# Performance work log

Measured on AMD Instinct MI355X. Metric: run time of the kernel, lower is better.

Reference implementation:

```python
import jax, jax.numpy as jnp
import numpy as np

# ---- Cl(4,1) geometric-product Cayley table (32 blades, metric diag(+,+,+,+,-)) ----
def _build_gp_map():
    metric = [1.0, 1.0, 1.0, 1.0, -1.0]  # e1..e4 square to +1, e5 squares to -1
    gp = np.zeros((32, 32, 32), dtype=np.float32)
    for a in range(32):          # blade a as a bitmask over 5 generators
        for b in range(32):
            # sign from reordering generators into canonical order
            swaps = 0
            t = a >> 1
            while t:
                swaps += bin(t & b).count('1')
                t >>= 1
            sign = -1.0 if (swaps & 1) else 1.0
            # sign from contracted (repeated) generators via the metric
            common = a & b
            for i in range(5):
                if common & (1 << i):
                    sign *= metric[i]
            gp[a, b, a ^ b] = sign  # e_a * e_b = sign * e_{a xor b}
    return gp

GP_MAP = _build_gp_map()  # [32, 32, 32], highly sparse (one nonzero per (a,b))
EPS = 1e-6

B, S, IN, OUT = 2, 1024, 256, 256

def setup_inputs() -> dict:
    key = jax.random.key(0)
    k1, k2 = jax.random.split(key)
    x = jax.random.normal(k1, (B, S, IN, 32), dtype=jnp.float32)
    std = 1.0 / float(np.sqrt(IN * 32))  # grade-aware Xavier scale from reset_parameters
    weight = jax.random.normal(k2, (OUT, IN, 32), dtype=jnp.float32) * std
    return {"x": x, "weight": weight}

def normalize_cl41(mv):
    # normalize each multivector by its coefficient magnitude over the 32 lanes
    norm = jnp.sqrt(jnp.sum(mv * mv, axis=-1, keepdims=True) + EPS)
    return mv / norm

def reference(x, weight):
    gp = jnp.asarray(GP_MAP, dtype=x.dtype)
    # W_op[o,i,l,k] = sum_j weight[o,i,j] * gp[j,l,k]
    W_op = jnp.einsum('oij,jlk->oilk', weight, gp)
    # out[b,s,o,k] = sum_{i,l} x[b,s,i,l] * W_op[o,i,l,k]
    out = jnp.einsum('bsil,oilk->bsok', x, W_op)
    return normalize_cl41(out)
```

## Files before the change

### kernel.cpp

```cpp
#include <hip/hip_runtime.h>
#include <hip/hip_bf16.h>
#include <stdint.h>

typedef _Float16 f16;
typedef __attribute__((ext_vector_type(8))) _Float16 f16x8;
typedef __attribute__((ext_vector_type(4))) float f32x4;

#define M_DIM 2048
#define K_FULL 8192
#define M2 8192
#define K2 2048
#define N2 2048
#define BM 128
#define BN 128
#define BK 32
#define PSTR 132

struct CMat { int re[4][4]; int im[4][4]; };

constexpr CMat cmul(const CMat& A, const CMat& B) {
  CMat C{};
  for (int r = 0; r < 4; ++r)
    for (int c = 0; c < 4; ++c) {
      int re = 0, im = 0;
      for (int t = 0; t < 4; ++t) {
        re += A.re[r][t] * B.re[t][c] - A.im[r][t] * B.im[t][c];
        im += A.re[r][t] * B.im[t][c] + A.im[r][t] * B.re[t][c];
      }
      C.re[r][c] = re; C.im[r][c] = im;
    }
  return C;
}

constexpr int gp_sign_ct(int a, int b) {
  int sw = 0;
  for (int t = a >> 1; t; t >>= 1) {
    int x = t & b;
    while (x) { sw += x & 1; x >>= 1; }
  }
  int s = (sw & 1) ? -1 : 1;
  if ((a & b) & 16) s = -s;
  return s;
}

struct Tables {
  int8_t f_idx[32][4]; int8_t f_sgn[32][4];
  int8_t g_idx[32][4]; int8_t g_sgn[32][4];
  bool ok;
};

constexpr Tables make_tables() {
  CMat G[5] = {
    { {{0,0,0,1},{0,0,1,0},{0,1,0,0},{1,0,0,0}},
      {{0,0,0,0},{0,0,0,0},{0,0,0,0},{0,0,0,0}} },
    { {{0,0,0,0},{0,0,0,0},{0,0,0,0},{0,0,0,0}},
      {{0,0,0,-1},{0,0,1,0},{0,-1,0,0},{1,0,0,0}} },
    { {{0,0,1,0},{0,0,0,-1},{1,0,0,0},{0,-1,0,0}},
      {{0,0,0,0},{0,0,0,0},{0,0,0,0},{0,0,0,0}} },
    { {{0,0,0,0},{0,0,0,0},{0,0,0,0},{0,0,0,0}},
      {{0,0,-1,0},{0,0,0,-1},{1,0,0,0},{0,1,0,0}} },
    { {{0,0,0,0},{0,0,0,0},{0,0,0,0},{0,0,0,0}},
      {{1,0,0,0},{0,1,0,0},{0,0,-1,0},{0,0,0,-1}} } };
  CMat ID{ {{1,0,0,0},{0,1,0,0},{0,0,1,0},{0,0,0,1}},
           {{0,0,0,0},{0,0,0,0},{0,0,0,0},{0,0,0,0}} };
  CMat U[32] = {};
  for (int A = 0; A < 32; ++A) {
    CMat u = ID;
    for (int b = 0; b < 5; ++b) if (A & (1 << b)) u = cmul(u, G[b]);
    U[A] = u;
  }
  bool ok = true;
  for (int a = 0; a < 32; ++a)
    for (int b = 0; b < 32; ++b) {
      CMat P = cmul(U[a], U[b]);
      int s = gp_sign_ct(a, b);
      const CMat& T = U[a ^ b];
      for (int r = 0; r < 4; ++r)
        for (int c = 0; c < 4; ++c)
          if (P.re[r][c] != s * T.re[r][c] || P.im[r][c] != s * T.im[r][c]) ok = false;
    }
  Tables t{};
  int cnt[32] = {};
  for (int A = 0; A < 32; ++A) {
    int n = 0;
    for (int r = 0; r < 4; ++r)
      for (int c = 0; c < 4; ++c) {
        int vr = U[A].re[r][c], vi = U[A].im[r][c];
        if (vr) {
          int s = (r * 4 + c) * 2;
          if (n < 4 && cnt[s] < 4) {
            t.g_idx[A][n] = (int8_t)s; t.g_sgn[A][n] = (int8_t)vr;
            t.f_idx[s][cnt[s]] = (int8_t)A; t.f_sgn[s][cnt[s]] = (int8_t)vr;
            cnt[s]++;
          } else ok = false;
          n++;
        }
        if (vi) {
          int s = (r * 4 + c) * 2 + 1;
          if (n < 4 && cnt[s] < 4) {
            t.g_idx[A][n] = (int8_t)s; t.g_sgn[A][n] = (int8_t)vi;
            t.f_idx[s][cnt[s]] = (int8_t)A; t.f_sgn[s][cnt[s]] = (int8_t)vi;
            cnt[s]++;
          } else ok = false;
          n++;
        }
      }
    if (n != 4) ok = false;
  }
  for (int s = 0; s < 32; ++s) if (cnt[s] != 4) ok = false;
  t.ok = ok;
  return t;
}

constexpr Tables HT = make_tables();
static_assert(HT.ok, "Cl(4,1) -> M(4,C) homomorphism check FAILED");


__device__ __forceinline__ void async16(const f16* g, f16* l) {
  __builtin_amdgcn_global_load_lds(
      (const __attribute__((address_space(1))) uint32_t*)g,
      (__attribute__((address_space(3))) uint32_t*)l,
      16, 0, 0);
}

__device__ __forceinline__ float gp_sign_rt(int a, int b) {
  int sw = 0;
  for (int t = a >> 1; t; t >>= 1) sw += __popc(t & b);
  float s = (sw & 1) ? -1.0f : 1.0f;
  if ((a & b) & 16) s = -s;
  return s;
}

__global__ __launch_bounds__(256) void fwd_x_kernel(const float* __restrict__ x,
                                                    f16* __restrict__ Ag) {
  __shared__ float xs[256 * 33];
  const int m = blockIdx.x, t = threadIdx.x;
  const float4* src = (const float4*)(x + (size_t)m * 8192);
#pragma unroll
  for (int c = t; c < 2048; c += 256) {
    float4 v = src[c];
    float* d = xs + (c >> 3) * 33 + ((c & 7) << 2);
    d[0] = v.x; d[1] = v.y; d[2] = v.z; d[3] = v.w;
  }
  __syncthreads();
  const float* xv = xs + t * 33;
  float sv[32];
#pragma unroll
  for (int s = 0; s < 32; ++s)
    sv[s] = (float)HT.f_sgn[s][0] * xv[HT.f_idx[s][0]]
          + (float)HT.f_sgn[s][1] * xv[HT.f_idx[s][1]]
          + (float)HT.f_sgn[s][2] * xv[HT.f_idx[s][2]]
          + (float)HT.f_sgn[s][3] * xv[HT.f_idx[s][3]];
#pragma unroll
  for (int c = 0; c < 4; ++c) {
    f16x8 h;
#pragma unroll
    for (int e = 0; e < 8; ++e) {
      int tt = e >> 1, p = e & 1;
      h[e] = (f16)sv[tt * 8 + c * 2 + p];
    }
    *(f16x8*)(Ag + ((size_t)(m * 4 + c)) * K2 + t * 8) = h;
  }
}

__global__ __launch_bounds__(256) void fwd_w_kernel(const float* __restrict__ w,
                                                    f16* __restrict__ Bt) {
  __shared__ float xs[256 * 33];
  const int o = blockIdx.x, t = threadIdx.x;
  const float4* src = (const float4*)(w + (size_t)o * 8192);
#pragma unroll
  for (int c = t; c < 2048; c += 256) {
    float4 v = src[c];
    float* d = xs + (c >> 3) * 33 + ((c & 7) << 2);
    d[0] = v.x; d[1] = v.y; d[2] = v.z; d[3] = v.w;
  }
  __syncthreads();
  const float* wv = xs + t * 33;
  float sv[32];
#pragma unroll
  for (int s = 0; s < 32; ++s)
    sv[s] = (float)HT.f_sgn[s][0] * wv[HT.f_idx[s][0]]
          + (float)HT.f_sgn[s][1] * wv[HT.f_idx[s][1]]
          + (float)HT.f_sgn[s][2] * wv[HT.f_idx[s][2]]
          + (float)HT.f_sgn[s][3] * wv[HT.f_idx[s][3]];
#pragma unroll
  for (int r = 0; r < 4; ++r)
#pragma unroll
    for (int q = 0; q < 2; ++q) {
      f16x8 h;
#pragma unroll
      for (int e = 0; e < 8; ++e) {
        int tt = e >> 1, p = e & 1;
        float re = sv[(r * 4 + tt) * 2], im = sv[(r * 4 + tt) * 2 + 1];
        float v = (q == 0) ? (p == 0 ? re : -im) : (p == 0 ? im : re);
        h[e] = (f16)v;
      }
      *(f16x8*)(Bt + ((size_t)(o * 8 + r * 2 + q)) * K2 + t * 8) = h;
    }
}

__global__ __launch_bounds__(256) void gemm_fused_kernel(const f16* __restrict__ A,
                                                         const f16* __restrict__ Bw,
                                                         float* __restrict__ out) {
  __shared__ __align__(16) char smem[64 * PSTR * 4];
  f16* As = (f16*)smem;
  f16* Bs = (f16*)(smem + BM * BK * 2);
  float* ps = (float*)smem;
  const int t = threadIdx.x;
  const int wave = t >> 6, lane = t & 63;
  const int wr = wave >> 1, wc = wave & 1;
  const int g = lane >> 4, lc = lane & 15;
  const int m0 = blockIdx.y * BM, n0 = blockIdx.x * BN;

  f32x4 acc[4][4];
#pragma unroll
  for (int i = 0; i < 4; ++i)
#pragma unroll
    for (int j = 0; j < 4; ++j) {
      acc[i][j][0] = 0.f; acc[i][j][1] = 0.f; acc[i][j][2] = 0.f; acc[i][j][3] = 0.f;
    }

  const f16* agp[2]; const f16* bgp[2];
  f16* alp[2]; f16* blp[2];
#pragma unroll
  for (int q = 0; q < 2; ++q) {
    int chunk = (q << 8) + (wave << 6) + lane;
    int row = chunk >> 2;
    int gk = ((chunk & 3) ^ ((row >> 1) & 3)) << 3;
    agp[q] = A  + (size_t)(m0 + row) * K2 + gk;
    bgp[q] = Bw + (size_t)(n0 + row) * K2 + gk;
    alp[q] = As + (q << 11) + (wave << 9);
    blp[q] = Bs + (q << 11) + (wave << 9);
  }

  const int swz = (lc >> 1) & 3;
  int aoff[4], boff[4];
#pragma unroll
  for (int i = 0; i < 4; ++i) {
    aoff[i] = ((wr << 6) + (i << 4) + lc) * BK + ((g ^ swz) << 3);
    boff[i] = ((wc << 6) + (i << 4) + lc) * BK + ((g ^ swz) << 3);
  }

  for (int kk = 0; kk < K2; kk += BK) {
    async16(agp[0] + kk, alp[0]);
    async16(agp[1] + kk, alp[1]);
    async16(bgp[0] + kk, blp[0]);
    async16(bgp[1] + kk, blp[1]);
    __syncthreads();

    f16x8 av[4], bv[4];
#pragma unroll
    for (int i = 0; i < 4; ++i) av[i] = *(const f16x8*)(As + aoff[i]);
#pragma unroll
    for (int i = 0; i < 4; ++i) bv[i] = *(const f16x8*)(Bs + boff[i]);
#pragma unroll
    for (int tm = 0; tm < 4; ++tm)
#pragma unroll
      for (int tn = 0; tn < 4; ++tn)
        acc[tm][tn] = __builtin_amdgcn_mfma_f32_16x16x32_f16(av[tm], bv[tn],
                                                             acc[tm][tn], 0, 0, 0);
    __syncthreads();
  }

#pragma unroll
  for (int half = 0; half < 2; ++half) {
    if (half) __syncthreads();
    if (wr == half) {
#pragma unroll
      for (int tm = 0; tm < 4; ++tm) {
        int rowl = (tm << 4) + (g << 2);
#pragma unroll
        for (int tn = 0; tn < 4; ++tn) {
          int col = (wc << 6) + (tn << 4) + lc;
#pragma unroll
          for (int r = 0; r < 4; ++r)
            ps[(rowl + r) * PSTR + col] = acc[tm][tn][r];
        }
      }
    }
    __syncthreads();

    const int mh = t >> 4, oh = t & 15;
    float yv[4][8];
#pragma unroll
    for (int c = 0; c < 4; ++c) {
      const float* row = ps + (mh * 4 + c) * PSTR + oh * 8;
      *(float4*)&yv[c][0] = *(const float4*)row;
      *(float4*)&yv[c][4] = *(const float4*)(row + 4);
    }
    float ss = 0.f;
#pragma unroll
    for (int c = 0; c < 4; ++c)
#pragma unroll
      for (int j = 0; j < 8; ++j) ss += yv[c][j] * yv[c][j];
    float inv = rsqrtf(0.25f * ss + 1e-6f);

    float ov[32];
#pragma unroll
    for (int k = 0; k < 32; ++k) {
      float v = 0.f;
#pragma unroll
      for (int j = 0; j < 4; ++j) {
        int s = HT.g_idx[k][j];
        int cell = s >> 1;
        int rr = cell >> 2, cc = cell & 3, pp = s & 1;
        float sgn = (float)HT.g_sgn[k][j];
        v += sgn * yv[cc][rr * 2 + pp];
      }
      ov[k] = v * 0.25f * inv;
    }
    int m = (m0 >> 2) + (half << 4) + mh;
    int o = (n0 >> 3) + oh;
    float* op = out + (size_t)m * 8192 + o * 32;
#pragma unroll
    for (int q = 0; q < 8; ++q)
      *(float4*)(op + q * 4) = make_float4(ov[q * 4], ov[q * 4 + 1],
                                           ov[q * 4 + 2], ov[q * 4 + 3]);
  }
}

__global__ __launch_bounds__(256) void naive_vl_kernel(const float* __restrict__ x,
                                                       const float* __restrict__ w,
                                                       float* __restrict__ out) {
  __shared__ float xs[8192];
  __shared__ float sgt[1024];
  int m = blockIdx.x, o0 = blockIdx.y << 3;
  int t = threadIdx.x;
  for (int i = t; i < 1024; i += 256) {
    int kk = i >> 5, ll = i & 31;
    sgt[i] = gp_sign_rt(kk ^ ll, ll);
  }
  const float4* xr = (const float4*)(x + (size_t)m * K_FULL);
  float4* xs4 = (float4*)xs;
  for (int i = t; i < 2048; i += 256) xs4[i] = xr[i];
  __syncthreads();
  int k = t & 31, ol = t >> 5;
  int o = o0 + ol;
  const float* wrow = w + (size_t)o * K_FULL;
  float acc = 0.f;
  for (int l = 0; l < 32; ++l) {
    float s = sgt[(k << 5) + l];
    const float* wp = wrow + (k ^ l);
    const float* xp = xs + l;
    float part = 0.f;
#pragma unroll 8
    for (int i = 0; i < 256; ++i) part += xp[i << 5] * wp[i << 5];
    acc += part * s;
  }
  float ss = acc * acc;
  for (int msk = 1; msk < 32; msk <<= 1) ss += __shfl_xor(ss, msk, 32);
  out[((size_t)m * 256 + o) * 32 + k] = acc * rsqrtf(ss + 1e-6f);
}

extern "C" void kernel_launch(void* const* d_in, const int* in_sizes, int n_in,
                              void* d_out, int out_size, void* d_ws, size_t ws_size,
                              hipStream_t stream) {
  const float* x = (const float*)d_in[0];
  const float* w = (const float*)d_in[1];
  float* out = (float*)d_out;

  size_t agE = (size_t)M2 * K2;
  size_t btE = (size_t)N2 * K2;
  size_t need = (agE + btE) * sizeof(f16);

  if (ws_size >= need) {
    f16* Ag = (f16*)d_ws;
    f16* Bt = Ag + agE;
    fwd_x_kernel<<<dim3(M_DIM), dim3(256), 0, stream>>>(x, Ag);
    fwd_w_kernel<<<dim3(256), dim3(256), 0, stream>>>(w, Bt);
    gemm_fused_kernel<<<dim3(N2 / BN, M2 / BM), dim3(256), 0, stream>>>(Ag, Bt, out);
  } else {
    naive_vl_kernel<<<dim3(M_DIM, 32), dim3(256), 0, stream>>>(x, w, out);
  }
}
```

Before: 233.1 us.

## Rewrite GEMM as 256x256 double-buffered MFMA pipeline with block swizzle

Grows the fused GEMM tile to 256x256x64 with 512 threads and 8 waves, and double-buffers the 128KB LDS so the global-to-LDS async loads for tile t+2 overlap the MFMAs on tile t. Manual vmcnt waits, raw s_barrier, setprio and sched_barrier phases interleave LDS fragment reads with the MFMA groups. A 1D grid with a block-index swizzle is meant to improve L2 reuse. The aim is to cut global traffic per flop and hide load latency. In exchange it needs far more LDS and registers per block, which risks low occupancy, and the hand-written sync is fragile.

```diff
diff --git a/kernel.cpp b/kernel.cpp
--- a/kernel.cpp
+++ b/kernel.cpp
@@ -11,10 +11,11 @@
 #define M2 8192
 #define K2 2048
 #define N2 2048
-#define BM 128
-#define BN 128
-#define BK 32
-#define PSTR 132
+#define BM 256
+#define BN 256
+#define BK 64
+#define NT (K2 / BK)
+#define PSTR 260
 
 struct CMat { int re[4][4]; int im[4][4]; };
 
@@ -114,7 +115,7 @@
 
 constexpr Tables HT = make_tables();
 static_assert(HT.ok, "Cl(4,1) -> M(4,C) homomorphism check FAILED");
-
+static_assert((NT & 1) == 0, "buffer parity requires even tile count");
 
 __device__ __forceinline__ void async16(const f16* g, f16* l) {
   __builtin_amdgcn_global_load_lds(
@@ -130,6 +131,10 @@
   if ((a & b) & 16) s = -s;
   return s;
 }
+
+#define FENCE() asm volatile("" ::: "memory")
+#define BARRIER() do { FENCE(); __builtin_amdgcn_s_barrier(); FENCE(); } while (0)
+#define WAIT_VM(N) asm volatile("s_waitcnt vmcnt(" #N ")" ::: "memory")
 
 __global__ __launch_bounds__(256) void fwd_x_kernel(const float* __restrict__ x,
                                                     f16* __restrict__ Ag) {
@@ -199,88 +204,161 @@
     }
 }
 
-__global__ __launch_bounds__(256) void gemm_fused_kernel(const f16* __restrict__ A,
-                                                         const f16* __restrict__ Bw,
-                                                         float* __restrict__ out) {
-  __shared__ __align__(16) char smem[64 * PSTR * 4];
-  f16* As = (f16*)smem;
-  f16* Bs = (f16*)(smem + BM * BK * 2);
-  float* ps = (float*)smem;
+__global__ __launch_bounds__(512, 2) void gemm_fused_kernel(const f16* __restrict__ A,
+                                                            const f16* __restrict__ Bw,
+                                                            float* __restrict__ out) {
+  __shared__ __align__(16) char smem[131072];
   const int t = threadIdx.x;
-  const int wave = t >> 6, lane = t & 63;
-  const int wr = wave >> 1, wc = wave & 1;
+  const int w = t >> 6, lane = t & 63;
+  const int wr = w >> 2, wc = w & 3;
   const int g = lane >> 4, lc = lane & 15;
-  const int m0 = blockIdx.y * BM, n0 = blockIdx.x * BN;
-
-  f32x4 acc[4][4];
-#pragma unroll
-  for (int i = 0; i < 4; ++i)
+
+  const int bid = blockIdx.x;
+  const int swzb = (bid & 7) * 32 + (bid >> 3);
+  const int by = swzb >> 3, bx = swzb & 7;
+  const int m0 = by * BM, n0 = bx * BN;
+
+  const int srow = lane >> 3;
+  const int schk = (lane & 7) ^ srow;
+  const f16* ga0 = A  + (size_t)(m0 + w * 8 + srow) * K2 + schk * 8;
+  const f16* gb0 = Bw + (size_t)(n0 + w * 8 + srow) * K2 + schk * 8;
+  const int lw = w << 10;
+
+  const int cks0 = (g ^ (lc & 7)) << 4;
+  const int cks1 = ((4 | g) ^ (lc & 7)) << 4;
+  const int arow = (wr << 14) + (lc << 7);
+  const int brow = 32768 + (wc << 13) + (lc << 7);
+
+  f32x4 acc[8][4];
+#pragma unroll
+  for (int i = 0; i < 8; ++i)
 #pragma unroll
     for (int j = 0; j < 4; ++j) {
       acc[i][j][0] = 0.f; acc[i][j][1] = 0.f; acc[i][j][2] = 0.f; acc[i][j][3] = 0.f;
     }
 
-  const f16* agp[2]; const f16* bgp[2];
-  f16* alp[2]; f16* blp[2];
-#pragma unroll
-  for (int q = 0; q < 2; ++q) {
-    int chunk = (q << 8) + (wave << 6) + lane;
-    int row = chunk >> 2;
-    int gk = ((chunk & 3) ^ ((row >> 1) & 3)) << 3;
-    agp[q] = A  + (size_t)(m0 + row) * K2 + gk;
-    bgp[q] = Bw + (size_t)(n0 + row) * K2 + gk;
-    alp[q] = As + (q << 11) + (wave << 9);
-    blp[q] = Bs + (q << 11) + (wave << 9);
-  }
-
-  const int swz = (lc >> 1) & 3;
-  int aoff[4], boff[4];
-#pragma unroll
-  for (int i = 0; i < 4; ++i) {
-    aoff[i] = ((wr << 6) + (i << 4) + lc) * BK + ((g ^ swz) << 3);
-    boff[i] = ((wc << 6) + (i << 4) + lc) * BK + ((g ^ swz) << 3);
-  }
-
-  for (int kk = 0; kk < K2; kk += BK) {
-    async16(agp[0] + kk, alp[0]);
-    async16(agp[1] + kk, alp[1]);
-    async16(bgp[0] + kk, blp[0]);
-    async16(bgp[1] + kk, blp[1]);
-    __syncthreads();
-
-    f16x8 av[4], bv[4];
-#pragma unroll
-    for (int i = 0; i < 4; ++i) av[i] = *(const f16x8*)(As + aoff[i]);
-#pragma unroll
-    for (int i = 0; i < 4; ++i) bv[i] = *(const f16x8*)(Bs + boff[i]);
-#pragma unroll
-    for (int tm = 0; tm < 4; ++tm)
-#pragma unroll
-      for (int tn = 0; tn < 4; ++tn)
-        acc[tm][tn] = __builtin_amdgcn_mfma_f32_16x16x32_f16(av[tm], bv[tn],
-                                                             acc[tm][tn], 0, 0, 0);
-    __syncthreads();
-  }
-
-#pragma unroll
-  for (int half = 0; half < 2; ++half) {
-    if (half) __syncthreads();
-    if (wr == half) {
-#pragma unroll
-      for (int tm = 0; tm < 4; ++tm) {
-        int rowl = (tm << 4) + (g << 2);
+#define STAGE(bo, kko) do {                                              \
+    const int _k = (kko);                                                \
+    async16(ga0 + _k,          (f16*)(smem + (bo) + lw));                \
+    async16(ga0 + _k + 131072, (f16*)(smem + (bo) + 8192  + lw));        \
+    async16(ga0 + _k + 262144, (f16*)(smem + (bo) + 16384 + lw));        \
+    async16(ga0 + _k + 393216, (f16*)(smem + (bo) + 24576 + lw));        \
+    async16(gb0 + _k,          (f16*)(smem + (bo) + 32768 + lw));        \
+    async16(gb0 + _k + 131072, (f16*)(smem + (bo) + 40960 + lw));        \
+    async16(gb0 + _k + 262144, (f16*)(smem + (bo) + 49152 + lw));        \
+    async16(gb0 + _k + 393216, (f16*)(smem + (bo) + 57344 + lw));        \
+  } while (0)
+
+  STAGE(0, 0);
+  STAGE(65536, BK);
+  WAIT_VM(8);
+  BARRIER();
+
+  f16x8 av[4][2], bv[4][2];
+  for (int tt = 0; tt < NT; ++tt) {
+    const int bo = (tt & 1) << 16;
+    const char* ab = smem + bo + arow;
+    const char* bb = smem + bo + brow;
+
+#pragma unroll
+    for (int i = 0; i < 4; ++i) {
+      av[i][0] = *(const f16x8*)(ab + i * 2048 + cks0);
+      av[i][1] = *(const f16x8*)(ab + i * 2048 + cks1);
+    }
+#pragma unroll
+    for (int j = 0; j < 2; ++j) {
+      bv[j][0] = *(const f16x8*)(bb + j * 2048 + cks0);
+      bv[j][1] = *(const f16x8*)(bb + j * 2048 + cks1);
+    }
+    __builtin_amdgcn_s_setprio(1);
+#pragma unroll
+    for (int k2 = 0; k2 < 2; ++k2)
+#pragma unroll
+      for (int i = 0; i < 4; ++i)
+#pragma unroll
+        for (int j = 0; j < 2; ++j)
+          acc[i][j] = __builtin_amdgcn_mfma_f32_16x16x32_f16(av[i][k2], bv[j][k2],
+                                                             acc[i][j], 0, 0, 0);
+    __builtin_amdgcn_s_setprio(0);
+    __builtin_amdgcn_sched_barrier(0);
+    BARRIER();
+
+#pragma unroll
+    for (int j = 2; j < 4; ++j) {
+      bv[j][0] = *(const f16x8*)(bb + j * 2048 + cks0);
+      bv[j][1] = *(const f16x8*)(bb + j * 2048 + cks1);
+    }
+    __builtin_amdgcn_s_setprio(1);
+#pragma unroll
+    for (int k2 = 0; k2 < 2; ++k2)
+#pragma unroll
+      for (int i = 0; i < 4; ++i)
+#pragma unroll
+        for (int j = 2; j < 4; ++j)
+          acc[i][j] = __builtin_amdgcn_mfma_f32_16x16x32_f16(av[i][k2], bv[j][k2],
+                                                             acc[i][j], 0, 0, 0);
+    __builtin_amdgcn_s_setprio(0);
+    __builtin_amdgcn_sched_barrier(0);
+    BARRIER();
+
+#pragma unroll
+    for (int i = 0; i < 4; ++i) {
+      av[i][0] = *(const f16x8*)(ab + (4 + i) * 2048 + cks0);
+      av[i][1] = *(const f16x8*)(ab + (4 + i) * 2048 + cks1);
+    }
+    __builtin_amdgcn_s_setprio(1);
+#pragma unroll
+    for (int k2 = 0; k2 < 2; ++k2)
+#pragma unroll
+      for (int i = 0; i < 4; ++i)
+#pragma unroll
+        for (int j = 0; j < 2; ++j)
+          acc[4 + i][j] = __builtin_amdgcn_mfma_f32_16x16x32_f16(av[i][k2], bv[j][k2],
+                                                                 acc[4 + i][j], 0, 0, 0);
+    __builtin_amdgcn_s_setprio(0);
+    __builtin_amdgcn_sched_barrier(0);
+    BARRIER();
+
+    if (tt + 2 < NT) STAGE(bo, (tt + 2) * BK);
+    __builtin_amdgcn_s_setprio(1);
+#pragma unroll
+    for (int k2 = 0; k2 < 2; ++k2)
+#pragma unroll
+      for (int i = 0; i < 4; ++i)
+#pragma unroll
+        for (int j = 2; j < 4; ++j)
+          acc[4 + i][j] = __builtin_amdgcn_mfma_f32_16x16x32_f16(av[i][k2], bv[j][k2],
+                                                                 acc[4 + i][j], 0, 0, 0);
+    __builtin_amdgcn_s_setprio(0);
+    __builtin_amdgcn_sched_barrier(0);
+    if (tt + 2 < NT) { WAIT_VM(8); }
+    else if (tt + 1 < NT) { WAIT_VM(0); }
+    BARRIER();
+  }
+#undef STAGE
+
+  float* ps = (float*)smem;
+  __syncthreads();
+#pragma unroll
+  for (int qq = 0; qq < 4; ++qq) {
+    if (qq) __syncthreads();
+    if (wr == (qq >> 1)) {
+      const int tb = (qq & 1) << 2;
+#pragma unroll
+      for (int tmi = 0; tmi < 4; ++tmi) {
+        const int rowl = tmi * 16 + g * 4;
 #pragma unroll
         for (int tn = 0; tn < 4; ++tn) {
-          int col = (wc << 6) + (tn << 4) + lc;
+          const int col = wc * 64 + tn * 16 + lc;
 #pragma unroll
           for (int r = 0; r < 4; ++r)
-            ps[(rowl + r) * PSTR + col] = acc[tm][tn][r];
+            ps[(rowl + r) * PSTR + col] = acc[tb + tmi][tn][r];
         }
       }
     }
     __syncthreads();
 
-    const int mh = t >> 4, oh = t & 15;
+    const int mh = t >> 5, oh = t & 31;
     float yv[4][8];
 #pragma unroll
     for (int c = 0; c < 4; ++c) {
@@ -309,13 +387,13 @@
       }
       ov[k] = v * 0.25f * inv;
     }
-    int m = (m0 >> 2) + (half << 4) + mh;
-    int o = (n0 >> 3) + oh;
+    int m = by * 64 + qq * 16 + mh;
+    int o = bx * 32 + oh;
     float* op = out + (size_t)m * 8192 + o * 32;
 #pragma unroll
-    for (int q = 0; q < 8; ++q)
-      *(float4*)(op + q * 4) = make_float4(ov[q * 4], ov[q * 4 + 1],
-                                           ov[q * 4 + 2], ov[q * 4 + 3]);
+    for (int qv = 0; qv < 8; ++qv)
+      *(float4*)(op + qv * 4) = make_float4(ov[qv * 4], ov[qv * 4 + 1],
+                                            ov[qv * 4 + 2], ov[qv * 4 + 3]);
   }
 }
 
@@ -368,7 +446,7 @@
     f16* Bt = Ag + agE;
     fwd_x_kernel<<<dim3(M_DIM), dim3(256), 0, stream>>>(x, Ag);
     fwd_w_kernel<<<dim3(256), dim3(256), 0, stream>>>(w, Bt);
-    gemm_fused_kernel<<<dim3(N2 / BN, M2 / BM), dim3(256), 0, stream>>>(Ag, Bt, out);
+    gemm_fused_kernel<<<dim3((M2 / BM) * (N2 / BN)), dim3(512), 0, stream>>>(Ag, Bt, out);
   } else {
     naive_vl_kernel<<<dim3(M_DIM, 32), dim3(256), 0, stream>>>(x, w, out);
   }
```

After: 195.5 us. 16.1% less time.
